# Optimization experiments

Hardware: AMD Instinct MI355X
Metric: run time of the kernel (lower is better)

Reference implementation:

```python
import jax, jax.numpy as jnp
import numpy as np

EPS = 1e-8


def setup_inputs() -> dict:
    key = jax.random.key(0)
    ks = jax.random.split(key, 8)
    B, N, D = 8, 1024, 256
    x = jax.random.normal(ks[0], (B, N, D), dtype=jnp.float32)
    y = jax.random.normal(ks[1], (B, N, D), dtype=jnp.float32)
    coords = jax.random.normal(ks[2], (N, N, 6), dtype=jnp.float32)
    # xavier-ish init for U, kaiming-ish for S1/S2
    U = jax.random.normal(ks[3], (D, D), dtype=jnp.float32) * (1.0 / np.sqrt(D))
    S1 = jax.random.normal(ks[4], (D, 1), dtype=jnp.float32)
    S2 = jax.random.normal(ks[5], (D, 1), dtype=jnp.float32)
    gating = jnp.asarray(1.0, dtype=jnp.float32)
    h_temp = jnp.asarray(0.1, dtype=jnp.float32)
    p_temp = jnp.asarray(1.0, dtype=jnp.float32)
    # trunc_normal_(a=0, b=1): std-normal truncated to [0, 1]
    pos_emb = jax.random.truncated_normal(ks[6], 0.0, 1.0, (N, 6, 1)).astype(jnp.float32)
    return {"x": x, "y": y, "coords": coords, "U": U, "S1": S1, "S2": S2,
            "gating": gating, "h_temp": h_temp, "p_temp": p_temp, "pos_emb": pos_emb}


def _spectral(x, U, S):
    # x @ U.T @ diag(|S|) @ U  ==  ((x @ U.T) * |S|) @ U
    s = jnp.abs(S[:, 0])
    return ((x @ U.T) * s) @ U


def reference(x, y, coords, U, S1, S2, gating, h_temp, p_temp, pos_emb):
    B, N, D = x.shape
    scale = D ** (-0.5)
    xs = jnp.stack([_spectral(x, U, S1), _spectral(x, U, S2)], axis=1)  # [B,2,N,D]
    # patch attention scores: [B,2,N,N]
    patch_score = jax.nn.softmax(jnp.einsum('bknd,bmd->bknm', xs, y) * scale, axis=-1)
    # positional scores, shared across batch and the 2 spectral branches: [N,N]
    pos_logits = -jnp.abs(p_temp) * jnp.einsum('nmc,ncq->nm', coords, pos_emb)
    pos_score = jax.nn.softmax(pos_logits, axis=-1)
    g = jax.nn.sigmoid(gating)
    attn = (1.0 - g) * patch_score + g * pos_score[None, None]  # [B,2,N,N]
    # entropy over key axis -> [B,N,2]
    entropy = jnp.sum(-attn * jnp.log(attn + EPS), axis=-1).transpose(0, 2, 1)
    hmap = 2.0 - 2.0 * jax.nn.sigmoid(h_temp * entropy)  # [B,N,2]
    fgbg = hmap[..., 0] >= hmap[..., 1]
    route = jax.lax.stop_gradient(
        jnp.stack([fgbg, ~fgbg], axis=-1).astype(hmap.dtype))  # [B,N,2]
    heat_map = jnp.sum(hmap * route, axis=-1, keepdims=True)  # [B,N,1]
    attn_sel = jnp.sum(attn * route.transpose(0, 2, 1)[..., None], axis=1)  # [B,N,N]
    out = attn_sel @ y  # [B,N,D]
    return (out, heat_map)
```

## Files before the change

### kernel.cpp

```cpp
#include <hip/hip_runtime.h>
#include <hip/hip_bf16.h>
#include <stdint.h>


#define NB 8
#define NN_ 1024
#define ND 256

typedef __bf16 bf16x8 __attribute__((ext_vector_type(8)));
typedef __bf16 bf16x4 __attribute__((ext_vector_type(4)));
typedef float f32x4 __attribute__((ext_vector_type(4)));

__device__ inline void gl_lds(const __bf16* g, __bf16* l) {
    auto gp = (const __attribute__((address_space(1))) uint32_t*)(uintptr_t)g;
    auto lp = (__attribute__((address_space(3))) uint32_t*)(uintptr_t)l;
    __builtin_amdgcn_global_load_lds(gp, lp, 16, 0, 0);
}

__device__ inline float wred_sum(float v) {
#pragma unroll
    for (int o = 32; o; o >>= 1) v += __shfl_xor(v, o, 64);
    return v;
}
__device__ inline float wred_max(float v) {
#pragma unroll
    for (int o = 32; o; o >>= 1) v = fmaxf(v, __shfl_xor(v, o, 64));
    return v;
}
__device__ inline float bred_sum(float v, float* red) {
    v = wred_sum(v);
    int w = threadIdx.x >> 6;
    __syncthreads();
    if ((threadIdx.x & 63) == 0) red[w] = v;
    __syncthreads();
    return red[0] + red[1] + red[2] + red[3];
}
__device__ inline float bred_max(float v, float* red) {
    v = wred_max(v);
    int w = threadIdx.x >> 6;
    __syncthreads();
    if ((threadIdx.x & 63) == 0) red[w] = v;
    __syncthreads();
    return fmaxf(fmaxf(red[0], red[1]), fmaxf(red[2], red[3]));
}

__global__ __launch_bounds__(256) void pos_kernel(
    const float* __restrict__ coords, const float* __restrict__ pos_emb,
    const float* __restrict__ p_temp, float* __restrict__ posS) {
    __shared__ float red[4];
    const int n = blockIdx.x;
    const int tid = threadIdx.x;
    const float pt = -fabsf(p_temp[0]);
    float pe[6];
#pragma unroll
    for (int c = 0; c < 6; ++c) pe[c] = pos_emb[n * 6 + c];
    const float* cr = coords + (long)n * NN_ * 6;
    float l[4];
#pragma unroll
    for (int j = 0; j < 4; ++j) {
        const int m = j * 256 + tid;
        const float2* cp = (const float2*)(cr + (long)m * 6);
        float2 c0 = cp[0], c1 = cp[1], c2 = cp[2];
        l[j] = pt * (c0.x * pe[0] + c0.y * pe[1] + c1.x * pe[2] +
                     c1.y * pe[3] + c2.x * pe[4] + c2.y * pe[5]);
    }
    float mx = fmaxf(fmaxf(l[0], l[1]), fmaxf(l[2], l[3]));
    mx = bred_max(mx, red);
    float e[4], s = 0.f;
#pragma unroll
    for (int j = 0; j < 4; ++j) { e[j] = expf(l[j] - mx); s += e[j]; }
    s = bred_sum(s, red);
    const float inv = 1.f / s;
#pragma unroll
    for (int j = 0; j < 4; ++j) posS[(long)n * NN_ + j * 256 + tid] = e[j] * inv;
}

__global__ __launch_bounds__(256) void conv_split(
    const float* __restrict__ src, __bf16* __restrict__ hi,
    __bf16* __restrict__ lo, int n4) {
    int i = blockIdx.x * 256 + threadIdx.x;
    const int stride = gridDim.x * 256;
    for (; i < n4; i += stride) {
        float4 v = ((const float4*)src)[i];
        bf16x4 h, l;
        h[0] = (__bf16)v.x; l[0] = (__bf16)(v.x - (float)h[0]);
        h[1] = (__bf16)v.y; l[1] = (__bf16)(v.y - (float)h[1]);
        h[2] = (__bf16)v.z; l[2] = (__bf16)(v.z - (float)h[2]);
        h[3] = (__bf16)v.w; l[3] = (__bf16)(v.w - (float)h[3]);
        ((bf16x4*)hi)[i] = h;
        ((bf16x4*)lo)[i] = l;
    }
}

__global__ __launch_bounds__(256) void build_M(
    const float* __restrict__ U, const float* __restrict__ S1,
    const float* __restrict__ S2, __bf16* __restrict__ Mh,
    __bf16* __restrict__ Ml) {
    const int n = blockIdx.x, j = threadIdx.x;
    float a1 = 0.f, a2 = 0.f;
    for (int c = 0; c < ND; ++c) {
        const float un = U[c * ND + n];
        const float uj = U[c * ND + j];
        a1 = fmaf(fabsf(S1[c]) * un, uj, a1);
        a2 = fmaf(fabsf(S2[c]) * un, uj, a2);
    }
    const __bf16 h1 = (__bf16)a1, h2 = (__bf16)a2;
    Mh[n * ND + j] = h1;            Ml[n * ND + j] = (__bf16)(a1 - (float)h1);
    Mh[65536 + n * ND + j] = h2;    Ml[65536 + n * ND + j] = (__bf16)(a2 - (float)h2);
}

__global__ __launch_bounds__(256) void prep_y(
    const float* __restrict__ y, __bf16* __restrict__ yt,
    __bf16* __restrict__ Yh, __bf16* __restrict__ Yl) {
    __shared__ __bf16 t[64][72];
    const int b = blockIdx.z;
    const int m0 = blockIdx.x * 64, d0 = blockIdx.y * 64;
    const int tid = threadIdx.x;
    const int c = tid & 15;
    const int r = tid >> 4;
#pragma unroll
    for (int p = 0; p < 4; ++p) {
        const int row = r + p * 16;
        const long gi = ((long)b * NN_ + m0 + row) * ND + d0 + c * 4;
        float4 v = *(const float4*)(y + gi);
        bf16x4 h, l;
        h[0] = (__bf16)v.x; l[0] = (__bf16)(v.x - (float)h[0]);
        h[1] = (__bf16)v.y; l[1] = (__bf16)(v.y - (float)h[1]);
        h[2] = (__bf16)v.z; l[2] = (__bf16)(v.z - (float)h[2]);
        h[3] = (__bf16)v.w; l[3] = (__bf16)(v.w - (float)h[3]);
        *(bf16x4*)(Yh + gi) = h;
        *(bf16x4*)(Yl + gi) = l;
        t[c * 4 + 0][row] = h[0]; t[c * 4 + 1][row] = h[1];
        t[c * 4 + 2][row] = h[2]; t[c * 4 + 3][row] = h[3];
    }
    __syncthreads();
#pragma unroll
    for (int p = 0; p < 4; ++p) {
        const int d = r + p * 16;
        bf16x4 o;
        o[0] = t[d][c * 4 + 0]; o[1] = t[d][c * 4 + 1];
        o[2] = t[d][c * 4 + 2]; o[3] = t[d][c * 4 + 3];
        *(bf16x4*)(yt + ((long)b * ND + d0 + d) * NN_ + m0 + c * 4) = o;
    }
}

template <int BN, bool SPLIT, int OUTM>
__global__ __launch_bounds__(256) void mgemm(
    const __bf16* __restrict__ Ah, const __bf16* __restrict__ Al,
    const __bf16* __restrict__ Bh, const __bf16* __restrict__ Bl,
    float* __restrict__ C, __bf16* __restrict__ Ch, __bf16* __restrict__ Cl,
    int M, int N, int K,
    long sA1, long sA2, int divA, long sB1, int divB, long sC, float alpha) {
    constexpr int BM = 128, BK = 32;
    constexpr int NBUF = SPLIT ? 2 : 1;
    constexpr int NF = BN / 32;
    __shared__ __bf16 As[NBUF * BM * BK];
    __shared__ __bf16 Bs[NBUF * BN * BK];

    const int z = blockIdx.z;
    const long aoff = (long)(z / divA) * sA1 + (long)(z % divA) * sA2;
    const long boff = (long)(z / divB) * sB1;
    Ah += aoff; if (SPLIT) Al += aoff;
    Bh += boff; if (SPLIT) Bl += boff;

    const int tid = threadIdx.x;
    const int bm = blockIdx.y * BM, bn = blockIdx.x * BN;
    const int wave = tid >> 6, lane = tid & 63;
    const int wm = wave >> 1, wn = wave & 1;
    const int quad = lane >> 4, l16 = lane & 15;

    f32x4 acc[4][NF];
#pragma unroll
    for (int i = 0; i < 4; ++i)
#pragma unroll
        for (int j = 0; j < NF; ++j) acc[i][j] = (f32x4){0.f, 0.f, 0.f, 0.f};

    const int srow = lane >> 2;
    const int slot = lane & 3;

    for (int k0 = 0; k0 < K; k0 += BK) {
        __syncthreads();
#pragma unroll
        for (int i = 0; i < 2; ++i) {
            const int r0 = wave * 32 + i * 16;
            const int row = r0 + srow;
            const int chunk = slot ^ ((row >> 1) & 3);
            const long g = (long)(bm + row) * K + k0 + chunk * 8;
            gl_lds(Ah + g, &As[r0 * 32]);
            if (SPLIT) gl_lds(Al + g, &As[BM * BK + r0 * 32]);
        }
        if (BN == 128) {
#pragma unroll
            for (int i = 0; i < 2; ++i) {
                const int r0 = wave * 32 + i * 16;
                const int row = r0 + srow;
                const int chunk = slot ^ ((row >> 1) & 3);
                const long g = (long)(bn + row) * K + k0 + chunk * 8;
                gl_lds(Bh + g, &Bs[r0 * 32]);
                if (SPLIT) gl_lds(Bl + g, &Bs[BN * BK + r0 * 32]);
            }
        } else {
            const int r0 = wave * 16;
            const int row = r0 + srow;
            const int chunk = slot ^ ((row >> 1) & 3);
            const long g = (long)(bn + row) * K + k0 + chunk * 8;
            gl_lds(Bh + g, &Bs[r0 * 32]);
            if (SPLIT) gl_lds(Bl + g, &Bs[BN * BK + r0 * 32]);
        }
        __syncthreads();

        bf16x8 a_h[4], a_l[4], b_h[NF], b_l[NF];
#pragma unroll
        for (int mi = 0; mi < 4; ++mi) {
            const int row = wm * 64 + mi * 16 + l16;
            const int off = row * 32 + ((quad ^ ((row >> 1) & 3)) * 8);
            a_h[mi] = *(const bf16x8*)&As[off];
            if (SPLIT) a_l[mi] = *(const bf16x8*)&As[BM * BK + off];
        }
#pragma unroll
        for (int ni = 0; ni < NF; ++ni) {
            const int row = wn * (BN / 2) + ni * 16 + l16;
            const int off = row * 32 + ((quad ^ ((row >> 1) & 3)) * 8);
            b_h[ni] = *(const bf16x8*)&Bs[off];
            if (SPLIT) b_l[ni] = *(const bf16x8*)&Bs[BN * BK + off];
        }
#pragma unroll
        for (int mi = 0; mi < 4; ++mi)
#pragma unroll
            for (int ni = 0; ni < NF; ++ni) {
                acc[mi][ni] = __builtin_amdgcn_mfma_f32_16x16x32_bf16(
                    a_h[mi], b_h[ni], acc[mi][ni], 0, 0, 0);
                if (SPLIT) {
                    acc[mi][ni] = __builtin_amdgcn_mfma_f32_16x16x32_bf16(
                        a_h[mi], b_l[ni], acc[mi][ni], 0, 0, 0);
                    acc[mi][ni] = __builtin_amdgcn_mfma_f32_16x16x32_bf16(
                        a_l[mi], b_h[ni], acc[mi][ni], 0, 0, 0);
                }
            }
    }

    C += (long)z * sC; Ch += (long)z * sC; Cl += (long)z * sC;
#pragma unroll
    for (int mi = 0; mi < 4; ++mi) {
        const int row0 = bm + wm * 64 + mi * 16 + quad * 4;
#pragma unroll
        for (int ni = 0; ni < NF; ++ni) {
            const int col = bn + wn * (BN / 2) + ni * 16 + l16;
#pragma unroll
            for (int r = 0; r < 4; ++r) {
                const float v = acc[mi][ni][r] * alpha;
                const long idx = (long)(row0 + r) * N + col;
                if (OUTM == 0) {
                    C[idx] = v;
                } else {
                    const __bf16 h = (__bf16)v;
                    Ch[idx] = h;
                    Cl[idx] = (__bf16)(v - (float)h);
                }
            }
        }
    }
}

__global__ __launch_bounds__(256) void blend_kernel(
    const float* __restrict__ S, const float* __restrict__ pos,
    const float* __restrict__ gating, const float* __restrict__ h_temp,
    float* __restrict__ heat, __bf16* __restrict__ Pb) {
    __shared__ float red[4];
    const int bn = blockIdx.x;
    const int b = bn >> 10, n = bn & 1023;
    const float* S0 = S + ((long)(b * 2 + 0) * NN_ + n) * NN_;
    const float* S1 = S + ((long)(b * 2 + 1) * NN_ + n) * NN_;
    const int tid = threadIdx.x;

    float4 l0 = *(const float4*)(S0 + tid * 4);
    float4 l1 = *(const float4*)(S1 + tid * 4);
    float4 pv = *(const float4*)(pos + (long)n * NN_ + tid * 4);

    float m0 = fmaxf(fmaxf(l0.x, l0.y), fmaxf(l0.z, l0.w));
    m0 = bred_max(m0, red);
    float e0x = expf(l0.x - m0), e0y = expf(l0.y - m0),
          e0z = expf(l0.z - m0), e0w = expf(l0.w - m0);
    float s0 = bred_sum(e0x + e0y + e0z + e0w, red);
    const float i0 = 1.f / s0;
    float m1 = fmaxf(fmaxf(l1.x, l1.y), fmaxf(l1.z, l1.w));
    m1 = bred_max(m1, red);
    float e1x = expf(l1.x - m1), e1y = expf(l1.y - m1),
          e1z = expf(l1.z - m1), e1w = expf(l1.w - m1);
    float s1 = bred_sum(e1x + e1y + e1z + e1w, red);
    const float i1 = 1.f / s1;

    const float g = 1.f / (1.f + expf(-gating[0]));
    const float cg = 1.f - g;

    float a0[4], a1[4];
    a0[0] = cg * (e0x * i0) + g * pv.x; a0[1] = cg * (e0y * i0) + g * pv.y;
    a0[2] = cg * (e0z * i0) + g * pv.z; a0[3] = cg * (e0w * i0) + g * pv.w;
    a1[0] = cg * (e1x * i1) + g * pv.x; a1[1] = cg * (e1y * i1) + g * pv.y;
    a1[2] = cg * (e1z * i1) + g * pv.z; a1[3] = cg * (e1w * i1) + g * pv.w;

    float ent0 = 0.f, ent1 = 0.f;
#pragma unroll
    for (int j = 0; j < 4; ++j) {
        ent0 -= a0[j] * logf(a0[j] + 1e-8f);
        ent1 -= a1[j] * logf(a1[j] + 1e-8f);
    }
    ent0 = bred_sum(ent0, red);
    ent1 = bred_sum(ent1, red);

    const float ht = h_temp[0];
    const float hm0 = 2.f - 2.f / (1.f + expf(-ht * ent0));
    const float hm1 = 2.f - 2.f / (1.f + expf(-ht * ent1));
    const bool fg = (hm0 >= hm1);
    if (tid == 0) heat[bn] = fg ? hm0 : hm1;

    bf16x4 o;
    o[0] = (__bf16)(fg ? a0[0] : a1[0]);
    o[1] = (__bf16)(fg ? a0[1] : a1[1]);
    o[2] = (__bf16)(fg ? a0[2] : a1[2]);
    o[3] = (__bf16)(fg ? a0[3] : a1[3]);
    *(bf16x4*)(Pb + ((long)b * NN_ + n) * NN_ + tid * 4) = o;
}

extern "C" void kernel_launch(void* const* d_in, const int* in_sizes, int n_in,
                              void* d_out, int out_size, void* d_ws, size_t ws_size,
                              hipStream_t stream) {
    const float* x      = (const float*)d_in[0];
    const float* y      = (const float*)d_in[1];
    const float* coords = (const float*)d_in[2];
    const float* U      = (const float*)d_in[3];
    const float* S1p    = (const float*)d_in[4];
    const float* S2p    = (const float*)d_in[5];
    const float* gating = (const float*)d_in[6];
    const float* h_temp = (const float*)d_in[7];
    const float* p_temp = (const float*)d_in[8];
    const float* pos_emb= (const float*)d_in[9];

    float* out  = (float*)d_out;
    float* heat = out + (long)NB * NN_ * ND;

    char* ws = (char*)d_ws;
    const long MB = 1 << 20;
    float*  Sf  = (float*)(ws);
    float*  pos = (float*)(ws + 64 * MB);
    __bf16* Xh  = (__bf16*)(ws + 68 * MB);
    __bf16* Xl  = (__bf16*)(ws + 72 * MB);
    __bf16* XSh = (__bf16*)(ws + 76 * MB);
    __bf16* XSl = (__bf16*)(ws + 84 * MB);
    __bf16* Pb  = (__bf16*)(ws + 68 * MB);
    __bf16* yt  = (__bf16*)(ws + 92 * MB);
    __bf16* Yh  = (__bf16*)(ws + 96 * MB);
    __bf16* Yl  = (__bf16*)(ws + 100 * MB);
    __bf16* Mh  = (__bf16*)(ws + 104 * MB);
    __bf16* Ml  = Mh + 2 * 65536;

    const long ND2 = (long)NN_ * ND;
    const long BND = (long)NB * ND2;

    pos_kernel<<<dim3(NN_), 256, 0, stream>>>(coords, pos_emb, p_temp, pos);
    conv_split<<<dim3(2048), 256, 0, stream>>>(x, Xh, Xl, (int)(BND / 4));
    prep_y<<<dim3(16, 4, NB), 256, 0, stream>>>(y, yt, Yh, Yl);
    build_M<<<dim3(ND), ND, 0, stream>>>(U, S1p, S2p, Mh, Ml);

    mgemm<64, true, 1><<<dim3(4, 64, 2), 256, 0, stream>>>(
        Xh, Xl, Mh, Ml, nullptr, XSh, XSl, NB * NN_, ND, ND,
        0, 0, 1, 65536, 1, BND, 1.0f);

    mgemm<128, true, 0><<<dim3(8, 8, NB * 2), 256, 0, stream>>>(
        XSh, XSl, Yh, Yl, Sf, nullptr, nullptr, NN_, NN_, ND,
        ND2, BND, 2, ND2, 2, (long)NN_ * NN_, 0.0625f);

    blend_kernel<<<dim3(NB * NN_), 256, 0, stream>>>(Sf, pos, gating, h_temp, heat, Pb);

    mgemm<64, false, 0><<<dim3(4, 8, NB), 256, 0, stream>>>(
        Pb, nullptr, yt, nullptr, out, nullptr, nullptr, NN_, ND, NN_,
        (long)NN_ * NN_, 0, 1, ND2, 1, ND2, 1.0f);

    (void)in_sizes; (void)n_in; (void)out_size; (void)ws_size;
}
```

Before: 220.5 us.

## Fuse score GEMM, softmax blend, entropy routing and output GEMM into one kernel

Replaces the score GEMM, the per-row blend kernel and the output GEMM with one kernel. Each block computes full 1024-wide score rows for 32 queries in registers, does the softmax, positional blend, entropy and route selection in place, stages the selected bf16 probabilities in LDS, then multiplies by y. This removes the 64MB fp32 score matrix write and read and the bf16 probability round trip through global memory. The cost is very heavy register use (256 accumulator floats per thread), occupancy limited to one block per CU, and operands read straight from global memory without LDS tiling. It also switches to the fast __expf/__logf intrinsics.

```diff
diff --git a/kernel.cpp b/kernel.cpp
--- a/kernel.cpp
+++ b/kernel.cpp
@@ -262,64 +262,273 @@
     }
 }
 
-__global__ __launch_bounds__(256) void blend_kernel(
-    const float* __restrict__ S, const float* __restrict__ pos,
+__global__ __launch_bounds__(256, 1) void mega_kernel(
+    const __bf16* __restrict__ XSh, const __bf16* __restrict__ XSl,
+    const __bf16* __restrict__ Yh, const __bf16* __restrict__ Yl,
+    const __bf16* __restrict__ yt, const float* __restrict__ pos,
     const float* __restrict__ gating, const float* __restrict__ h_temp,
-    float* __restrict__ heat, __bf16* __restrict__ Pb) {
-    __shared__ float red[4];
-    const int bn = blockIdx.x;
-    const int b = bn >> 10, n = bn & 1023;
-    const float* S0 = S + ((long)(b * 2 + 0) * NN_ + n) * NN_;
-    const float* S1 = S + ((long)(b * 2 + 1) * NN_ + n) * NN_;
+    float* __restrict__ heat, float* __restrict__ out) {
+    extern __shared__ char smem[];
+    __bf16* Pl  = (__bf16*)smem;
+    float* red0 = (float*)(smem + 66048);
+    float* red1 = red0 + 256;
+    float* red2 = red1 + 256;
+
+    const int b  = blockIdx.x & 7;
+    const int n0 = (blockIdx.x >> 3) * 32;
     const int tid = threadIdx.x;
-
-    float4 l0 = *(const float4*)(S0 + tid * 4);
-    float4 l1 = *(const float4*)(S1 + tid * 4);
-    float4 pv = *(const float4*)(pos + (long)n * NN_ + tid * 4);
-
-    float m0 = fmaxf(fmaxf(l0.x, l0.y), fmaxf(l0.z, l0.w));
-    m0 = bred_max(m0, red);
-    float e0x = expf(l0.x - m0), e0y = expf(l0.y - m0),
-          e0z = expf(l0.z - m0), e0w = expf(l0.w - m0);
-    float s0 = bred_sum(e0x + e0y + e0z + e0w, red);
-    const float i0 = 1.f / s0;
-    float m1 = fmaxf(fmaxf(l1.x, l1.y), fmaxf(l1.z, l1.w));
-    m1 = bred_max(m1, red);
-    float e1x = expf(l1.x - m1), e1y = expf(l1.y - m1),
-          e1z = expf(l1.z - m1), e1w = expf(l1.w - m1);
-    float s1 = bred_sum(e1x + e1y + e1z + e1w, red);
-    const float i1 = 1.f / s1;
-
-    const float g = 1.f / (1.f + expf(-gating[0]));
+    const int wave = tid >> 6, lane = tid & 63;
+    const int quad = lane >> 4, l16 = lane & 15;
+    const int wcol = wave * 256;
+
+    const __bf16* Ahp = XSh + ((long)b * NN_ + n0) * ND;
+    const __bf16* Alp = XSl + ((long)b * NN_ + n0) * ND;
+    const __bf16* Bhp = Yh + ((long)b * NN_ + wcol) * ND;
+    const __bf16* Blp = Yl + ((long)b * NN_ + wcol) * ND;
+
+    f32x4 acc[2][2][16];
+#pragma unroll
+    for (int br = 0; br < 2; ++br)
+#pragma unroll
+        for (int mi = 0; mi < 2; ++mi)
+#pragma unroll
+            for (int ni = 0; ni < 16; ++ni)
+                acc[br][mi][ni] = (f32x4){0.f, 0.f, 0.f, 0.f};
+
+    for (int k0 = 0; k0 < ND; k0 += 32) {
+        bf16x8 ah[2][2], al[2][2];
+#pragma unroll
+        for (int br = 0; br < 2; ++br)
+#pragma unroll
+            for (int mi = 0; mi < 2; ++mi) {
+                const long o = (long)br * (NB * NN_ * ND) +
+                               (long)(mi * 16 + l16) * ND + k0 + quad * 8;
+                ah[br][mi] = *(const bf16x8*)(Ahp + o);
+                al[br][mi] = *(const bf16x8*)(Alp + o);
+            }
+#pragma unroll
+        for (int ni = 0; ni < 16; ++ni) {
+            const long o = (long)(ni * 16 + l16) * ND + k0 + quad * 8;
+            bf16x8 bh = *(const bf16x8*)(Bhp + o);
+            bf16x8 bl = *(const bf16x8*)(Blp + o);
+#pragma unroll
+            for (int br = 0; br < 2; ++br)
+#pragma unroll
+                for (int mi = 0; mi < 2; ++mi) {
+                    acc[br][mi][ni] = __builtin_amdgcn_mfma_f32_16x16x32_bf16(
+                        ah[br][mi], bh, acc[br][mi][ni], 0, 0, 0);
+                    acc[br][mi][ni] = __builtin_amdgcn_mfma_f32_16x16x32_bf16(
+                        ah[br][mi], bl, acc[br][mi][ni], 0, 0, 0);
+                    acc[br][mi][ni] = __builtin_amdgcn_mfma_f32_16x16x32_bf16(
+                        al[br][mi], bh, acc[br][mi][ni], 0, 0, 0);
+                }
+        }
+    }
+
+#pragma unroll
+    for (int br = 0; br < 2; ++br)
+#pragma unroll
+        for (int mi = 0; mi < 2; ++mi)
+#pragma unroll
+            for (int ni = 0; ni < 16; ++ni)
+#pragma unroll
+                for (int rr = 0; rr < 4; ++rr)
+                    acc[br][mi][ni][rr] *= 0.0625f;
+
+    float mx[2][2][4];
+#pragma unroll
+    for (int br = 0; br < 2; ++br)
+#pragma unroll
+        for (int mi = 0; mi < 2; ++mi)
+#pragma unroll
+            for (int rr = 0; rr < 4; ++rr) {
+                float m = -3.4e38f;
+#pragma unroll
+                for (int ni = 0; ni < 16; ++ni) m = fmaxf(m, acc[br][mi][ni][rr]);
+                mx[br][mi][rr] = m;
+            }
+#pragma unroll
+    for (int o = 1; o < 16; o <<= 1)
+#pragma unroll
+        for (int br = 0; br < 2; ++br)
+#pragma unroll
+            for (int mi = 0; mi < 2; ++mi)
+#pragma unroll
+                for (int rr = 0; rr < 4; ++rr)
+                    mx[br][mi][rr] = fmaxf(mx[br][mi][rr],
+                                           __shfl_xor(mx[br][mi][rr], o, 64));
+    if (l16 == 0)
+#pragma unroll
+        for (int br = 0; br < 2; ++br)
+#pragma unroll
+            for (int mi = 0; mi < 2; ++mi)
+#pragma unroll
+                for (int rr = 0; rr < 4; ++rr)
+                    red0[(wave * 2 + br) * 32 + mi * 16 + quad * 4 + rr] = mx[br][mi][rr];
+    __syncthreads();
+#pragma unroll
+    for (int br = 0; br < 2; ++br)
+#pragma unroll
+        for (int mi = 0; mi < 2; ++mi)
+#pragma unroll
+            for (int rr = 0; rr < 4; ++rr) {
+                const int ri = mi * 16 + quad * 4 + rr;
+                float m = red0[(0 * 2 + br) * 32 + ri];
+                m = fmaxf(m, red0[(1 * 2 + br) * 32 + ri]);
+                m = fmaxf(m, red0[(2 * 2 + br) * 32 + ri]);
+                m = fmaxf(m, red0[(3 * 2 + br) * 32 + ri]);
+                mx[br][mi][rr] = m;
+            }
+
+    float sm[2][2][4];
+#pragma unroll
+    for (int br = 0; br < 2; ++br)
+#pragma unroll
+        for (int mi = 0; mi < 2; ++mi)
+#pragma unroll
+            for (int rr = 0; rr < 4; ++rr) {
+                float s = 0.f;
+#pragma unroll
+                for (int ni = 0; ni < 16; ++ni) {
+                    const float e = __expf(acc[br][mi][ni][rr] - mx[br][mi][rr]);
+                    acc[br][mi][ni][rr] = e;
+                    s += e;
+                }
+                sm[br][mi][rr] = s;
+            }
+#pragma unroll
+    for (int o = 1; o < 16; o <<= 1)
+#pragma unroll
+        for (int br = 0; br < 2; ++br)
+#pragma unroll
+            for (int mi = 0; mi < 2; ++mi)
+#pragma unroll
+                for (int rr = 0; rr < 4; ++rr)
+                    sm[br][mi][rr] += __shfl_xor(sm[br][mi][rr], o, 64);
+    if (l16 == 0)
+#pragma unroll
+        for (int br = 0; br < 2; ++br)
+#pragma unroll
+            for (int mi = 0; mi < 2; ++mi)
+#pragma unroll
+                for (int rr = 0; rr < 4; ++rr)
+                    red1[(wave * 2 + br) * 32 + mi * 16 + quad * 4 + rr] = sm[br][mi][rr];
+    __syncthreads();
+    float inv[2][2][4];
+#pragma unroll
+    for (int br = 0; br < 2; ++br)
+#pragma unroll
+        for (int mi = 0; mi < 2; ++mi)
+#pragma unroll
+            for (int rr = 0; rr < 4; ++rr) {
+                const int ri = mi * 16 + quad * 4 + rr;
+                const float s = red1[(0 * 2 + br) * 32 + ri] + red1[(1 * 2 + br) * 32 + ri] +
+                                red1[(2 * 2 + br) * 32 + ri] + red1[(3 * 2 + br) * 32 + ri];
+                inv[br][mi][rr] = 1.f / s;
+            }
+
+    const float g = 1.f / (1.f + __expf(-gating[0]));
     const float cg = 1.f - g;
-
-    float a0[4], a1[4];
-    a0[0] = cg * (e0x * i0) + g * pv.x; a0[1] = cg * (e0y * i0) + g * pv.y;
-    a0[2] = cg * (e0z * i0) + g * pv.z; a0[3] = cg * (e0w * i0) + g * pv.w;
-    a1[0] = cg * (e1x * i1) + g * pv.x; a1[1] = cg * (e1y * i1) + g * pv.y;
-    a1[2] = cg * (e1z * i1) + g * pv.z; a1[3] = cg * (e1w * i1) + g * pv.w;
-
-    float ent0 = 0.f, ent1 = 0.f;
-#pragma unroll
-    for (int j = 0; j < 4; ++j) {
-        ent0 -= a0[j] * logf(a0[j] + 1e-8f);
-        ent1 -= a1[j] * logf(a1[j] + 1e-8f);
-    }
-    ent0 = bred_sum(ent0, red);
-    ent1 = bred_sum(ent1, red);
+    float ent[2][2][4];
+#pragma unroll
+    for (int br = 0; br < 2; ++br)
+#pragma unroll
+        for (int mi = 0; mi < 2; ++mi)
+#pragma unroll
+            for (int rr = 0; rr < 4; ++rr) ent[br][mi][rr] = 0.f;
+#pragma unroll
+    for (int mi = 0; mi < 2; ++mi)
+#pragma unroll
+        for (int ni = 0; ni < 16; ++ni)
+#pragma unroll
+            for (int rr = 0; rr < 4; ++rr) {
+                const int ri = mi * 16 + quad * 4 + rr;
+                const float pv = pos[(long)(n0 + ri) * NN_ + wcol + ni * 16 + l16];
+#pragma unroll
+                for (int br = 0; br < 2; ++br) {
+                    const float a = cg * acc[br][mi][ni][rr] * inv[br][mi][rr] + g * pv;
+                    acc[br][mi][ni][rr] = a;
+                    ent[br][mi][rr] -= a * __logf(a + 1e-8f);
+                }
+            }
+#pragma unroll
+    for (int o = 1; o < 16; o <<= 1)
+#pragma unroll
+        for (int br = 0; br < 2; ++br)
+#pragma unroll
+            for (int mi = 0; mi < 2; ++mi)
+#pragma unroll
+                for (int rr = 0; rr < 4; ++rr)
+                    ent[br][mi][rr] += __shfl_xor(ent[br][mi][rr], o, 64);
+    if (l16 == 0)
+#pragma unroll
+        for (int br = 0; br < 2; ++br)
+#pragma unroll
+            for (int mi = 0; mi < 2; ++mi)
+#pragma unroll
+                for (int rr = 0; rr < 4; ++rr)
+                    red2[(wave * 2 + br) * 32 + mi * 16 + quad * 4 + rr] = ent[br][mi][rr];
+    __syncthreads();
 
     const float ht = h_temp[0];
-    const float hm0 = 2.f - 2.f / (1.f + expf(-ht * ent0));
-    const float hm1 = 2.f - 2.f / (1.f + expf(-ht * ent1));
-    const bool fg = (hm0 >= hm1);
-    if (tid == 0) heat[bn] = fg ? hm0 : hm1;
-
-    bf16x4 o;
-    o[0] = (__bf16)(fg ? a0[0] : a1[0]);
-    o[1] = (__bf16)(fg ? a0[1] : a1[1]);
-    o[2] = (__bf16)(fg ? a0[2] : a1[2]);
-    o[3] = (__bf16)(fg ? a0[3] : a1[3]);
-    *(bf16x4*)(Pb + ((long)b * NN_ + n) * NN_ + tid * 4) = o;
+    float fsel[2][4];
+#pragma unroll
+    for (int mi = 0; mi < 2; ++mi)
+#pragma unroll
+        for (int rr = 0; rr < 4; ++rr) {
+            const int ri = mi * 16 + quad * 4 + rr;
+            const float e0 = red2[0 * 32 + ri] + red2[2 * 32 + ri] +
+                             red2[4 * 32 + ri] + red2[6 * 32 + ri];
+            const float e1 = red2[1 * 32 + ri] + red2[3 * 32 + ri] +
+                             red2[5 * 32 + ri] + red2[7 * 32 + ri];
+            const float hm0 = 2.f - 2.f / (1.f + __expf(-ht * e0));
+            const float hm1 = 2.f - 2.f / (1.f + __expf(-ht * e1));
+            const bool fg = (hm0 >= hm1);
+            fsel[mi][rr] = fg ? 1.f : 0.f;
+            if (wave == 0 && l16 == 0)
+                heat[(long)b * NN_ + n0 + ri] = fg ? hm0 : hm1;
+        }
+#pragma unroll
+    for (int mi = 0; mi < 2; ++mi)
+#pragma unroll
+        for (int ni = 0; ni < 16; ++ni)
+#pragma unroll
+            for (int rr = 0; rr < 4; ++rr) {
+                const int ri = mi * 16 + quad * 4 + rr;
+                const float v = fsel[mi][rr] != 0.f ? acc[0][mi][ni][rr]
+                                                    : acc[1][mi][ni][rr];
+                Pl[ri * 1032 + wcol + ni * 16 + l16] = (__bf16)v;
+            }
+    __syncthreads();
+
+    f32x4 oacc[2][4];
+#pragma unroll
+    for (int mi = 0; mi < 2; ++mi)
+#pragma unroll
+        for (int nd = 0; nd < 4; ++nd) oacc[mi][nd] = (f32x4){0.f, 0.f, 0.f, 0.f};
+    const __bf16* Bo = yt + ((long)b * ND + wave * 64) * NN_;
+    for (int k0 = 0; k0 < NN_; k0 += 32) {
+        bf16x8 pa[2];
+#pragma unroll
+        for (int mi = 0; mi < 2; ++mi)
+            pa[mi] = *(const bf16x8*)&Pl[(mi * 16 + l16) * 1032 + k0 + quad * 8];
+#pragma unroll
+        for (int nd = 0; nd < 4; ++nd) {
+            bf16x8 bo = *(const bf16x8*)(Bo + (long)(nd * 16 + l16) * NN_ + k0 + quad * 8);
+#pragma unroll
+            for (int mi = 0; mi < 2; ++mi)
+                oacc[mi][nd] = __builtin_amdgcn_mfma_f32_16x16x32_bf16(
+                    pa[mi], bo, oacc[mi][nd], 0, 0, 0);
+        }
+    }
+#pragma unroll
+    for (int mi = 0; mi < 2; ++mi)
+#pragma unroll
+        for (int nd = 0; nd < 4; ++nd)
+#pragma unroll
+            for (int r = 0; r < 4; ++r)
+                out[((long)b * NN_ + n0 + mi * 16 + quad * 4 + r) * ND +
+                    wave * 64 + nd * 16 + l16] = oacc[mi][nd][r];
 }
 
 extern "C" void kernel_launch(void* const* d_in, const int* in_sizes, int n_in,
@@ -341,17 +550,15 @@
 
     char* ws = (char*)d_ws;
     const long MB = 1 << 20;
-    float*  Sf  = (float*)(ws);
-    float*  pos = (float*)(ws + 64 * MB);
-    __bf16* Xh  = (__bf16*)(ws + 68 * MB);
-    __bf16* Xl  = (__bf16*)(ws + 72 * MB);
-    __bf16* XSh = (__bf16*)(ws + 76 * MB);
-    __bf16* XSl = (__bf16*)(ws + 84 * MB);
-    __bf16* Pb  = (__bf16*)(ws + 68 * MB);
-    __bf16* yt  = (__bf16*)(ws + 92 * MB);
-    __bf16* Yh  = (__bf16*)(ws + 96 * MB);
-    __bf16* Yl  = (__bf16*)(ws + 100 * MB);
-    __bf16* Mh  = (__bf16*)(ws + 104 * MB);
+    float*  pos = (float*)(ws);
+    __bf16* Xh  = (__bf16*)(ws + 4 * MB);
+    __bf16* Xl  = (__bf16*)(ws + 8 * MB);
+    __bf16* XSh = (__bf16*)(ws + 12 * MB);
+    __bf16* XSl = (__bf16*)(ws + 20 * MB);
+    __bf16* yt  = (__bf16*)(ws + 28 * MB);
+    __bf16* Yh  = (__bf16*)(ws + 32 * MB);
+    __bf16* Yl  = (__bf16*)(ws + 36 * MB);
+    __bf16* Mh  = (__bf16*)(ws + 40 * MB);
     __bf16* Ml  = Mh + 2 * 65536;
 
     const long ND2 = (long)NN_ * ND;
@@ -366,15 +573,10 @@
         Xh, Xl, Mh, Ml, nullptr, XSh, XSl, NB * NN_, ND, ND,
         0, 0, 1, 65536, 1, BND, 1.0f);
 
-    mgemm<128, true, 0><<<dim3(8, 8, NB * 2), 256, 0, stream>>>(
-        XSh, XSl, Yh, Yl, Sf, nullptr, nullptr, NN_, NN_, ND,
-        ND2, BND, 2, ND2, 2, (long)NN_ * NN_, 0.0625f);
-
-    blend_kernel<<<dim3(NB * NN_), 256, 0, stream>>>(Sf, pos, gating, h_temp, heat, Pb);
-
-    mgemm<64, false, 0><<<dim3(4, 8, NB), 256, 0, stream>>>(
-        Pb, nullptr, yt, nullptr, out, nullptr, nullptr, NN_, ND, NN_,
-        (long)NN_ * NN_, 0, 1, ND2, 1, ND2, 1.0f);
+    hipFuncSetAttribute((const void*)mega_kernel,
+                        hipFuncAttributeMaxDynamicSharedMemorySize, 69632);
+    mega_kernel<<<dim3(256), 256, 69632, stream>>>(
+        XSh, XSl, Yh, Yl, yt, pos, gating, h_temp, heat, out);
 
     (void)in_sizes; (void)n_in; (void)out_size; (void)ws_size;
 }
```

Result: slower. 229.6 us (+4.1%).
